# Performance work log

Measured on AMD Instinct MI355X. Metric: run time of the kernel, lower is better.

The kernel has to match this reference:

```python
import jax, jax.numpy as jnp
import numpy as np

B, N, DIM, H = 4, 3072, 768, 3  # N must be 48*64 per positional-encoding assert; H must be 3 per reshape constraint
HD = DIM // H               # 256
D = HD + 6                  # per-head dim after positional concat


def _positional(n):
    # (x^2, y^2, xy, x, y, 1) encoding over a 48x64 grid, intrinsics=None path.
    h, w = 48, 64
    ys = jnp.linspace(-1.0, 1.0, h)
    xs = jnp.linspace(-1.0, 1.0, w)
    p3 = jnp.tile(ys, w)            # [N], ys.unsqueeze(0).repeat(B, w)
    p4 = jnp.repeat(xs, h)          # [N], xs.repeat_interleave(h)
    pos = jnp.stack([p3 * p3, p4 * p4, p3 * p4, p3, p4, jnp.ones_like(p3)], axis=-1)  # [N,6]
    return pos


def setup_inputs() -> dict:
    key = jax.random.key(0)
    k0, k1, k2 = jax.random.split(key, 3)
    x = jax.random.normal(k0, (B, N, DIM), dtype=jnp.float32)
    W_qkv = jax.random.normal(k1, (3 * DIM, DIM), dtype=jnp.float32) * (DIM ** -0.5)
    W_pf = jax.random.normal(k2, (DIM, DIM + 6 * H), dtype=jnp.float32) * ((DIM + 6 * H) ** -0.5)
    b_pf = jnp.zeros((DIM,), dtype=jnp.float32)
    return {"x": x, "W_qkv": W_qkv, "W_pf": W_pf, "b_pf": b_pf}


def reference(x, W_qkv, W_pf, b_pf):
    Bb, Nn, C = x.shape
    scale = HD ** -0.5
    qkv = (x @ W_qkv.T).reshape(Bb, Nn, 3, H, HD).transpose(2, 0, 3, 1, 4)  # [3,B,H,N,hd]
    q, k, v = qkv[0], qkv[1], qkv[2]
    attn = jnp.einsum('bhnd,bhmd->bhnm', q, k) * scale          # [B,H,N,N]
    attn_f = jax.nn.softmax(attn, axis=-1) * jax.nn.softmax(attn, axis=-2)
    pos = _positional(Nn)                                       # [N,6]
    pos_b = jnp.broadcast_to(pos[None, None], (Bb, H, Nn, 6))
    v_cat = jnp.concatenate([v, pos_b], axis=-1)                # [B,H,N,D]
    # fundamental = v^T @ attn_f @ v  -> [B,H,D,D]
    f1 = jnp.einsum('bhnd,bhnm->bhdm', v_cat, attn_f)
    fund = jnp.einsum('bhdm,bhme->bhde', f1, v_cat)
    # reshape [B,H,D,D] -> [B, 3D, D] -> transpose -> [B, D, 3D]
    fund = fund.reshape(Bb, H * D, D).transpose(0, 2, 1)
    out = fund @ W_pf.T + b_pf                                  # [B, D, DIM]
    return out
```

## Files before the change

### kernel.cpp

```cpp
#include <hip/hip_runtime.h>

typedef unsigned short u16;
typedef u16 u16x8 __attribute__((ext_vector_type(8)));
typedef u16 u16x4 __attribute__((ext_vector_type(4)));
typedef __bf16 bf16x8 __attribute__((ext_vector_type(8)));
typedef float f32x4 __attribute__((ext_vector_type(4)));

#define Bn   4
#define Nn   3072
#define DIMn 768
#define Hn   3
#define HDn  256
#define BHn  12
#define Dn   262
#define EP   272
#define MSn  8
#define FP   264

__device__ __forceinline__ u16 f2bf(float f) {
    unsigned u = __builtin_bit_cast(unsigned, f);
    u += 0x7fffu + ((u >> 16) & 1u);
    return (u16)(u >> 16);
}
__device__ __forceinline__ float bf2f(u16 h) {
    unsigned u = ((unsigned)h) << 16;
    return __builtin_bit_cast(float, u);
}
__device__ __forceinline__ bf16x8 ld_frag16(const u16* p) {
    return *(const bf16x8*)p;
}
#define MFMA(a,b,c) __builtin_amdgcn_mfma_f32_16x16x32_bf16(a, b, c, 0, 0, 0)

__global__ void to_bf16(const float* __restrict__ in, u16* __restrict__ out, int n8) {
    int i = blockIdx.x * blockDim.x + threadIdx.x;
    if (i >= n8) return;
    float4 a = *(const float4*)(in + (size_t)i*8);
    float4 b = *(const float4*)(in + (size_t)i*8 + 4);
    u16x8 o;
    o[0]=f2bf(a.x); o[1]=f2bf(a.y); o[2]=f2bf(a.z); o[3]=f2bf(a.w);
    o[4]=f2bf(b.x); o[5]=f2bf(b.y); o[6]=f2bf(b.z); o[7]=f2bf(b.w);
    *(u16x8*)(out + (size_t)i*8) = o;
}

__global__ __launch_bounds__(256) void transpose_wpf(const float* __restrict__ Wpf,
                                                     float* __restrict__ WpfT) {
    __shared__ float tile[32][33];
    int jt = blockIdx.x * 32;
    int ot = blockIdx.y * 32;
    int tx = threadIdx.x & 31, ty = threadIdx.x >> 5;
    #pragma unroll
    for (int k = 0; k < 4; ++k) {
        int o = ot + ty + 8*k;
        int j = jt + tx;
        tile[ty + 8*k][tx] = (j < 786) ? Wpf[(size_t)o*786 + j] : 0.0f;
    }
    __syncthreads();
    #pragma unroll
    for (int k = 0; k < 4; ++k) {
        int j = jt + ty + 8*k;
        if (j < 786) WpfT[(size_t)j*768 + ot + tx] = tile[tx][ty + 8*k];
    }
}

__global__ __launch_bounds__(256) void qkv_mfma(const u16* __restrict__ xb,
                                                const u16* __restrict__ Wb,
                                                u16* __restrict__ qh,
                                                u16* __restrict__ kh,
                                                u16* __restrict__ vT) {
    __shared__ u16 Pool[2*128*72];
    u16* Xs = Pool;
    u16* Ws = Pool + 128*72;
    int tid = threadIdx.x;
    int w = tid >> 6, lane = tid & 63, quad = lane >> 4, l15 = lane & 15;
    int cb = blockIdx.x, rb = blockIdx.y;
    int r0 = rb * 128;
    int b_ = rb / 24;
    int n0 = (rb % 24) * 128;
    int which = cb / 6;
    int c0l = (cb % 6) * 128;
    int h = c0l >> 8, hd0 = c0l & 255;
    int bh = b_ * Hn + h;
    int wr = w >> 1, wc = w & 1;
    const u16* xp = xb + (size_t)r0*DIMn;
    const u16* wp = Wb + (size_t)(which*768 + c0l)*DIMn;
    const int sr = tid >> 3, ssg = tid & 7;

    u16x8 xreg[4], wreg[4];
    #pragma unroll
    for (int i = 0; i < 4; ++i) {
        xreg[i] = *(const u16x8*)(xp + (size_t)(sr + 32*i)*DIMn + ssg*8);
        wreg[i] = *(const u16x8*)(wp + (size_t)(sr + 32*i)*DIMn + ssg*8);
    }

    f32x4 acc[4][4];
    #pragma unroll
    for (int i = 0; i < 4; ++i)
        #pragma unroll
        for (int j = 0; j < 4; ++j) acc[i][j] = (f32x4){0.f,0.f,0.f,0.f};

    for (int k0 = 0; k0 < DIMn; k0 += 64) {
        int k0n = (k0 + 64 < DIMn) ? k0 + 64 : 0;
        __syncthreads();
        #pragma unroll
        for (int i = 0; i < 4; ++i) {
            *(u16x8*)&Xs[(sr + 32*i)*72 + ssg*8] = xreg[i];
            *(u16x8*)&Ws[(sr + 32*i)*72 + ssg*8] = wreg[i];
        }
        __syncthreads();
        #pragma unroll
        for (int i = 0; i < 4; ++i) {
            xreg[i] = *(const u16x8*)(xp + (size_t)(sr + 32*i)*DIMn + k0n + ssg*8);
            wreg[i] = *(const u16x8*)(wp + (size_t)(sr + 32*i)*DIMn + k0n + ssg*8);
        }
        #pragma unroll
        for (int ks = 0; ks < 2; ++ks) {
            bf16x8 af[4], bf[4];
            #pragma unroll
            for (int mt = 0; mt < 4; ++mt)
                af[mt] = ld_frag16(&Xs[(wr*64 + mt*16 + l15)*72 + ks*32 + quad*8]);
            #pragma unroll
            for (int nt = 0; nt < 4; ++nt)
                bf[nt] = ld_frag16(&Ws[(wc*64 + nt*16 + l15)*72 + ks*32 + quad*8]);
            #pragma unroll
            for (int mt = 0; mt < 4; ++mt)
                #pragma unroll
                for (int nt = 0; nt < 4; ++nt)
                    acc[mt][nt] = MFMA(af[mt], bf[nt], acc[mt][nt]);
        }
    }
    __syncthreads();
    u16* Cw = Pool + w*(64*72);
    if (which < 2) {
        #pragma unroll
        for (int mt = 0; mt < 4; ++mt)
            #pragma unroll
            for (int nt = 0; nt < 4; ++nt)
                #pragma unroll
                for (int r = 0; r < 4; ++r)
                    Cw[(mt*16 + quad*4 + r)*72 + nt*16 + l15] = f2bf(acc[mt][nt][r]);
    } else {
        #pragma unroll
        for (int mt = 0; mt < 4; ++mt)
            #pragma unroll
            for (int nt = 0; nt < 4; ++nt) {
                u16x4 pk;
                #pragma unroll
                for (int r = 0; r < 4; ++r) pk[r] = f2bf(acc[mt][nt][r]);
                *(u16x4*)&Cw[(nt*16 + l15)*72 + mt*16 + quad*4] = pk;
            }
    }
    __syncthreads();
    #pragma unroll
    for (int i = 0; i < 8; ++i) {
        int u = tid + i*256;
        int row = u >> 4, seg = u & 15;
        if (which < 2) {
            int wv = ((row >> 6) << 1) | (seg >> 3);
            u16x8 vv = *(const u16x8*)&Pool[wv*(64*72) + (row & 63)*72 + (seg & 7)*8];
            u16* dst = (which == 0) ? qh : kh;
            *(u16x8*)(dst + ((size_t)bh*Nn + n0 + row)*HDn + hd0 + seg*8) = vv;
        } else {
            int wv = ((seg >> 3) << 1) | (row >> 6);
            u16x8 vv = *(const u16x8*)&Pool[wv*(64*72) + (row & 63)*72 + (seg & 7)*8];
            *(u16x8*)(vT + ((size_t)bh*EP + hd0 + row)*Nn + n0 + seg*8) = vv;
        }
    }
}

__global__ void pos_fill(u16* __restrict__ vT) {
    int idx = blockIdx.x * blockDim.x + threadIdx.x;
    int bh = idx / (16*Nn);
    int rem = idx - bh*16*Nn;
    int row = rem / Nn;
    int n = rem - row*Nn;
    int gy = n % 48, gx = n / 48;
    float p3 = -1.0f + (2.0f/47.0f)*gy;
    float p4 = -1.0f + (2.0f/63.0f)*gx;
    float v = 0.f;
    if (row == 0) v = p3*p3;
    else if (row == 1) v = p4*p4;
    else if (row == 2) v = p3*p4;
    else if (row == 3) v = p3;
    else if (row == 4) v = p4;
    else if (row == 5) v = 1.0f;
    vT[((size_t)bh*EP + 256 + row)*Nn + n] = f2bf(v);
}

__global__ __launch_bounds__(256) void rc_mfma(const u16* __restrict__ qh,
                                               const u16* __restrict__ kh,
                                               float* __restrict__ R_part,
                                               float* __restrict__ C_part,
                                               u16* __restrict__ P2,
                                               int g0) {
    __shared__ u16 Ks[64*264];
    __shared__ float rbuf[2][2][64];
    int tid = threadIdx.x;
    int w = tid >> 6, lane = tid & 63, quad = lane >> 4, l15 = lane & 15;
    int bhl = blockIdx.z;
    int bh = g0 + bhl;
    int nb = blockIdx.y;
    int n0 = nb * 64;
    int ms = blockIdx.x;
    int msBase = ms * (Nn/MSn);
    const u16* qp = qh + ((size_t)bh*Nn + n0)*HDn;
    const u16* kp = kh + (size_t)bh*Nn*HDn;
    u16* pw = P2 + (size_t)bhl*Nn*Nn;
    int wm = w & 1, wn = w >> 1;

    #pragma unroll
    for (int i = 0; i < 8; ++i) {
        int e = tid + i*256;
        int row = e >> 5, seg = e & 31;
        *(u16x8*)&Ks[row*264 + seg*8] = *(const u16x8*)(qp + (size_t)row*HDn + seg*8);
    }
    __syncthreads();
    bf16x8 qf[2][8];
    #pragma unroll
    for (int nt = 0; nt < 2; ++nt)
        #pragma unroll
        for (int ks = 0; ks < 8; ++ks)
            qf[nt][ks] = ld_frag16(&Ks[((2*wn+nt)*16 + l15)*264 + ks*32 + quad*8]);

    const int kr = tid >> 5, ksg = tid & 31;
    u16x8 kreg[8];
    #pragma unroll
    for (int i = 0; i < 8; ++i)
        kreg[i] = *(const u16x8*)(kp + (size_t)(msBase + kr + 8*i)*HDn + ksg*8);

    float* cpart = C_part + ((size_t)(nb*2 + wn)*BHn + bh)*Nn;
    float rAcc[2] = {0.f, 0.f};
    const int NCH = Nn/(MSn*64);
    for (int mc = 0; mc < NCH; ++mc) {
        int m0 = msBase + mc*64;
        int m0n = msBase + ((mc + 1 < NCH) ? (mc + 1)*64 : 0);
        __syncthreads();
        #pragma unroll
        for (int i = 0; i < 8; ++i)
            *(u16x8*)&Ks[(kr + 8*i)*264 + ksg*8] = kreg[i];
        __syncthreads();
        #pragma unroll
        for (int i = 0; i < 8; ++i)
            kreg[i] = *(const u16x8*)(kp + (size_t)(m0n + kr + 8*i)*HDn + ksg*8);
        f32x4 sacc[2][2];
        #pragma unroll
        for (int i = 0; i < 2; ++i)
            #pragma unroll
            for (int j = 0; j < 2; ++j) sacc[i][j] = (f32x4){0.f,0.f,0.f,0.f};
        #pragma unroll
        for (int ks = 0; ks < 8; ++ks) {
            bf16x8 a0 = ld_frag16(&Ks[((2*wm+0)*16 + l15)*264 + ks*32 + quad*8]);
            bf16x8 a1 = ld_frag16(&Ks[((2*wm+1)*16 + l15)*264 + ks*32 + quad*8]);
            sacc[0][0] = MFMA(a0, qf[0][ks], sacc[0][0]);
            sacc[0][1] = MFMA(a0, qf[1][ks], sacc[0][1]);
            sacc[1][0] = MFMA(a1, qf[0][ks], sacc[1][0]);
            sacc[1][1] = MFMA(a1, qf[1][ks], sacc[1][1]);
        }
        float ex[2][2][4];
        #pragma unroll
        for (int mt = 0; mt < 2; ++mt)
            #pragma unroll
            for (int nt = 0; nt < 2; ++nt)
                #pragma unroll
                for (int r = 0; r < 4; ++r)
                    ex[mt][nt][r] = __expf(0.0625f * sacc[mt][nt][r]);
        #pragma unroll
        for (int mt = 0; mt < 2; ++mt)
            #pragma unroll
            for (int nt = 0; nt < 2; ++nt) {
                u16x4 pk;
                #pragma unroll
                for (int r = 0; r < 4; ++r) {
                    float e2 = ex[mt][nt][r];
                    pk[r] = f2bf(e2 * e2);
                }
                *(u16x4*)(pw + (size_t)(n0 + (2*wn+nt)*16 + l15)*Nn
                             + m0 + (2*wm+mt)*16 + quad*4) = pk;
            }
        #pragma unroll
        for (int nt = 0; nt < 2; ++nt)
            #pragma unroll
            for (int mt = 0; mt < 2; ++mt)
                #pragma unroll
                for (int r = 0; r < 4; ++r) rAcc[nt] += ex[mt][nt][r];
        {
            float v0 = ex[0][0][0] + ex[0][1][0];
            float v1 = ex[0][0][1] + ex[0][1][1];
            float v2 = ex[0][0][2] + ex[0][1][2];
            float v3 = ex[0][0][3] + ex[0][1][3];
            float v4 = ex[1][0][0] + ex[1][1][0];
            float v5 = ex[1][0][1] + ex[1][1][1];
            float v6 = ex[1][0][2] + ex[1][1][2];
            float v7 = ex[1][0][3] + ex[1][1][3];
            int b0 = l15 & 1, b1 = l15 & 2, b2 = l15 & 4;
            float u01 = (b0 ? v1 : v0) + __shfl_xor(b0 ? v0 : v1, 1, 16);
            float u23 = (b0 ? v3 : v2) + __shfl_xor(b0 ? v2 : v3, 1, 16);
            float u45 = (b0 ? v5 : v4) + __shfl_xor(b0 ? v4 : v5, 1, 16);
            float u67 = (b0 ? v7 : v6) + __shfl_xor(b0 ? v6 : v7, 1, 16);
            float t03 = (b1 ? u23 : u01) + __shfl_xor(b1 ? u01 : u23, 2, 16);
            float t47 = (b1 ? u67 : u45) + __shfl_xor(b1 ? u45 : u67, 2, 16);
            float s07 = (b2 ? t47 : t03) + __shfl_xor(b2 ? t03 : t47, 4, 16);
            s07 += __shfl_xor(s07, 8, 16);
            if (l15 < 8)
                cpart[m0 + (2*wm + (l15 >> 2))*16 + quad*4 + (l15 & 3)] = s07;
        }
    }
    #pragma unroll
    for (int nt = 0; nt < 2; ++nt) {
        float rp = rAcc[nt];
        rp += __shfl_xor(rp, 16, 64);
        rp += __shfl_xor(rp, 32, 64);
        if (quad == 0) rbuf[wm][nt][wn*32 + l15] = rp;
    }
    __syncthreads();
    #pragma unroll
    for (int nt = 0; nt < 2; ++nt) {
        if (quad == 0 && wm == 0) {
            float tot = rbuf[0][nt][wn*32 + l15] + rbuf[1][nt][wn*32 + l15];
            R_part[(size_t)ms*BHn*Nn + (size_t)bh*Nn + n0 + (2*wn+nt)*16 + l15] = tot;
        }
    }
}

__global__ void inv_kernel(const float* __restrict__ Rg,
                           const float* __restrict__ Cg,
                           float* __restrict__ iRg, float* __restrict__ iCg) {
    int i = blockIdx.x * blockDim.x + threadIdx.x;
    float r = 0.f;
    #pragma unroll
    for (int s = 0; s < MSn; ++s)
        r += Rg[(size_t)s*BHn*Nn + i];
    float c = 0.f;
    for (int s = 0; s < 96; ++s)
        c += Cg[(size_t)s*BHn*Nn + i];
    iRg[i] = 1.0f / r;
    iCg[i] = 1.0f / c;
}

__global__ void scale_v(const u16* __restrict__ vTg, const float* __restrict__ iCg,
                        u16* __restrict__ vTs) {
    int idx = blockIdx.x * blockDim.x + threadIdx.x;
    int bhl = idx / (EP*Nn/8);
    int rem = idx - bhl*(EP*Nn/8);
    size_t off = (size_t)bhl*EP*Nn + (size_t)rem*8;
    int m = (rem % (Nn/8)) * 8;
    u16x8 v = *(const u16x8*)(vTg + off);
    float4 c0 = *(const float4*)(iCg + (size_t)bhl*Nn + m);
    float4 c1 = *(const float4*)(iCg + (size_t)bhl*Nn + m + 4);
    u16x8 o;
    o[0]=f2bf(bf2f(v[0])*c0.x); o[1]=f2bf(bf2f(v[1])*c0.y);
    o[2]=f2bf(bf2f(v[2])*c0.z); o[3]=f2bf(bf2f(v[3])*c0.w);
    o[4]=f2bf(bf2f(v[4])*c1.x); o[5]=f2bf(bf2f(v[5])*c1.y);
    o[6]=f2bf(bf2f(v[6])*c1.z); o[7]=f2bf(bf2f(v[7])*c1.w);
    *(u16x8*)(vTs + off) = o;
}

__global__ __launch_bounds__(256, 4) void pv_mfma(const u16* __restrict__ P2,
                                                  const u16* __restrict__ vTs,
                                                  const float* __restrict__ iRg,
                                                  u16* __restrict__ f1aTg) {
    __shared__ u16 Ps2[64*72];
    __shared__ u16 Vt[144*72];
    int tid = threadIdx.x;
    int w = tid >> 6, lane = tid & 63, quad = lane >> 4, l15 = lane & 15;
    int bhl = blockIdx.y, n0 = blockIdx.x * 64;
    int z = blockIdx.z;
    const u16* pp = P2  + ((size_t)bhl*Nn + n0)*Nn;
    const u16* vp = vTs + (size_t)bhl*EP*Nn + (size_t)(z*128)*Nn;
    const int sr = tid >> 3, sg = tid & 7;
    u16x8 preg[2], vreg[5];
    #pragma unroll
    for (int i = 0; i < 2; ++i)
        preg[i] = *(const u16x8*)(pp + (size_t)(sr + 32*i)*Nn + sg*8);
    #pragma unroll
    for (int i = 0; i < 5; ++i)
        if (i < 4 || (z == 1 && tid < 128))
            vreg[i] = *(const u16x8*)(vp + (size_t)(sr + 32*i)*Nn + sg*8);

    f32x4 acc[4][3];
    #pragma unroll
    for (int a = 0; a < 4; ++a)
        #pragma unroll
        for (int b = 0; b < 3; ++b) acc[a][b] = (f32x4){0.f,0.f,0.f,0.f};

    for (int mc = 0; mc < Nn/64; ++mc) {
        int m0n = (mc + 1 < Nn/64) ? (mc + 1)*64 : 0;
        __syncthreads();
        #pragma unroll
        for (int i = 0; i < 2; ++i)
            *(u16x8*)&Ps2[(sr + 32*i)*72 + sg*8] = preg[i];
        #pragma unroll
        for (int i = 0; i < 5; ++i)
            if (i < 4 || (z == 1 && tid < 128))
                *(u16x8*)&Vt[(sr + 32*i)*72 + sg*8] = vreg[i];
        __syncthreads();
        #pragma unroll
        for (int i = 0; i < 2; ++i)
            preg[i] = *(const u16x8*)(pp + (size_t)(sr + 32*i)*Nn + m0n + sg*8);
        #pragma unroll
        for (int i = 0; i < 5; ++i)
            if (i < 4 || (z == 1 && tid < 128))
                vreg[i] = *(const u16x8*)(vp + (size_t)(sr + 32*i)*Nn + m0n + sg*8);
        #pragma unroll
        for (int ks = 0; ks < 2; ++ks) {
            bf16x8 pa[4];
            #pragma unroll
            for (int nt = 0; nt < 4; ++nt)
                pa[nt] = ld_frag16(&Ps2[(nt*16 + l15)*72 + ks*32 + quad*8]);
            #pragma unroll
            for (int et = 0; et < 3; ++et) {
                const int lt = (et < 2) ? (w*2 + et) : 8;
                const bool act = (et < 2 || (z == 1 && w == 3));
                if (act) {
                    bf16x8 vb = ld_frag16(&Vt[(lt*16 + l15)*72 + ks*32 + quad*8]);
                    #pragma unroll
                    for (int nt = 0; nt < 4; ++nt)
                        acc[nt][et] = MFMA(pa[nt], vb, acc[nt][et]);
                }
            }
        }
    }
    #pragma unroll
    for (int nt = 0; nt < 4; ++nt) {
        float4 ir4 = *(const float4*)(iRg + (size_t)bhl*Nn + n0 + nt*16 + quad*4);
        #pragma unroll
        for (int et = 0; et < 3; ++et) {
            const int tile = (et < 2) ? (z*8 + w*2 + et) : 16;
            const bool act = (et < 2 || (z == 1 && w == 3));
            if (act) {
                int e = tile*16 + l15;
                u16x4 ov;
                #pragma unroll
                for (int r = 0; r < 4; ++r)
                    ov[r] = f2bf(acc[nt][et][r] * ((const float*)&ir4)[r]);
                *(u16x4*)(f1aTg + ((size_t)bhl*EP + e)*Nn + n0 + nt*16 + quad*4) = ov;
            }
        }
    }
}

__global__ __launch_bounds__(256) void fund_mfma(const u16* __restrict__ vT,
                                                 const u16* __restrict__ f1aT,
                                                 float* __restrict__ fund) {
    __shared__ u16 At[64*136];
    __shared__ u16 Bt[64*136];
    int tid = threadIdx.x;
    int w = tid >> 6, lane = tid & 63, quad = lane >> 4, l15 = lane & 15;
    int bh = blockIdx.z;
    int d0 = blockIdx.y * 64, e0 = blockIdx.x * 64;
    const u16* ap = vT   + (size_t)bh*EP*Nn;
    const u16* bp = f1aT + (size_t)bh*EP*Nn;
    int wd = w & 1, we = w >> 1;
    const u16x8 zero8 = {0,0,0,0,0,0,0,0};

    f32x4 acc[2][2];
    #pragma unroll
    for (int i = 0; i < 2; ++i)
        #pragma unroll
        for (int j = 0; j < 2; ++j) acc[i][j] = (f32x4){0.f,0.f,0.f,0.f};

    for (int nc = 0; nc < Nn; nc += 128) {
        __syncthreads();
        #pragma unroll
        for (int i = 0; i < 4; ++i) {
            int u = tid + i*256;
            int row = u >> 4, seg = u & 15;
            int da = d0 + row, eb = e0 + row;
            *(u16x8*)&At[row*136 + seg*8] = (da < EP)
                ? *(const u16x8*)(ap + (size_t)da*Nn + nc + seg*8) : zero8;
            *(u16x8*)&Bt[row*136 + seg*8] = (eb < EP)
                ? *(const u16x8*)(bp + (size_t)eb*Nn + nc + seg*8) : zero8;
        }
        __syncthreads();
        #pragma unroll
        for (int ks = 0; ks < 4; ++ks) {
            bf16x8 a0 = ld_frag16(&At[((2*wd+0)*16 + l15)*136 + ks*32 + quad*8]);
            bf16x8 a1 = ld_frag16(&At[((2*wd+1)*16 + l15)*136 + ks*32 + quad*8]);
            bf16x8 b0 = ld_frag16(&Bt[((2*we+0)*16 + l15)*136 + ks*32 + quad*8]);
            bf16x8 b1 = ld_frag16(&Bt[((2*we+1)*16 + l15)*136 + ks*32 + quad*8]);
            acc[0][0] = MFMA(a0, b0, acc[0][0]);
            acc[0][1] = MFMA(a0, b1, acc[0][1]);
            acc[1][0] = MFMA(a1, b0, acc[1][0]);
            acc[1][1] = MFMA(a1, b1, acc[1][1]);
        }
    }
    #pragma unroll
    for (int dt = 0; dt < 2; ++dt)
        #pragma unroll
        for (int et = 0; et < 2; ++et)
            #pragma unroll
            for (int r = 0; r < 4; ++r) {
                int d = d0 + (2*wd+dt)*16 + quad*4 + r;
                int e = e0 + (2*we+et)*16 + l15;
                if (d < Dn && e < Dn)
                    fund[(size_t)bh*Dn*FP + (size_t)d*FP + e] = acc[dt][et][r];
            }
}

__global__ __launch_bounds__(256) void out_gemm(const float* __restrict__ fund,
                                                const float* __restrict__ WpfT,
                                                const float* __restrict__ bpf,
                                                float* __restrict__ out) {
    __shared__ float As[2][16][68];
    __shared__ float Bs[2][16][68];
    int tid = threadIdx.x;
    int b_ = blockIdx.z;
    int d2b = blockIdx.y * 64, ob = blockIdx.x * 64;
    int ty = tid >> 4, tx = tid & 15;
    int srow = tid >> 4, sc4 = (tid & 15) * 4;
    const int NIT = (786 + 15) / 16;

    float4 aReg, bReg;
    {
        int j = srow;
        aReg = (float4){0.f,0.f,0.f,0.f};
        bReg = (float4){0.f,0.f,0.f,0.f};
        int h = j / Dn, d1 = j - h*Dn;
        const float* srcA = fund + ((size_t)(b_*Hn + h)*Dn + d1)*FP + d2b + sc4;
        if (d2b + sc4 + 3 < Dn) aReg = *(const float4*)srcA;
        else {
            float t[4] = {0.f,0.f,0.f,0.f};
            for (int u2 = 0; u2 < 4; ++u2)
                if (d2b + sc4 + u2 < Dn) t[u2] = srcA[u2];
            aReg = (float4){t[0],t[1],t[2],t[3]};
        }
        bReg = *(const float4*)(WpfT + (size_t)j*768 + ob + sc4);
    }
    *(float4*)&As[0][srow][sc4] = aReg;
    *(float4*)&Bs[0][srow][sc4] = bReg;
    __syncthreads();

    float acc[4][4] = {};
    for (int c = 0; c < NIT; ++c) {
        int buf = c & 1;
        if (c + 1 < NIT) {
            int j = (c + 1)*16 + srow;
            aReg = (float4){0.f,0.f,0.f,0.f};
            bReg = (float4){0.f,0.f,0.f,0.f};
            if (j < 786) {
                int h = j / Dn, d1 = j - h*Dn;
                const float* srcA = fund + ((size_t)(b_*Hn + h)*Dn + d1)*FP + d2b + sc4;
                if (d2b + sc4 + 3 < Dn) aReg = *(const float4*)srcA;
                else {
                    float t[4] = {0.f,0.f,0.f,0.f};
                    for (int u2 = 0; u2 < 4; ++u2)
                        if (d2b + sc4 + u2 < Dn) t[u2] = srcA[u2];
                    aReg = (float4){t[0],t[1],t[2],t[3]};
                }
                bReg = *(const float4*)(WpfT + (size_t)j*768 + ob + sc4);
            }
        }
        #pragma unroll
        for (int kk = 0; kk < 16; ++kk) {
            float4 a = *(const float4*)&As[buf][kk][ty*4];
            float4 b = *(const float4*)&Bs[buf][kk][tx*4];
            acc[0][0] += a.x*b.x; acc[0][1] += a.x*b.y; acc[0][2] += a.x*b.z; acc[0][3] += a.x*b.w;
            acc[1][0] += a.y*b.x; acc[1][1] += a.y*b.y; acc[1][2] += a.y*b.z; acc[1][3] += a.y*b.w;
            acc[2][0] += a.z*b.x; acc[2][1] += a.z*b.y; acc[2][2] += a.z*b.z; acc[2][3] += a.z*b.w;
            acc[3][0] += a.w*b.x; acc[3][1] += a.w*b.y; acc[3][2] += a.w*b.z; acc[3][3] += a.w*b.w;
        }
        if (c + 1 < NIT) {
            *(float4*)&As[buf^1][srow][sc4] = aReg;
            *(float4*)&Bs[buf^1][srow][sc4] = bReg;
            __syncthreads();
        }
    }
    #pragma unroll
    for (int i = 0; i < 4; ++i) {
        int d2 = d2b + ty*4 + i;
        if (d2 >= Dn) continue;
        #pragma unroll
        for (int j = 0; j < 4; ++j) {
            int o = ob + tx*4 + j;
            out[((size_t)b_*Dn + d2)*DIMn + o] = acc[i][j] + bpf[o];
        }
    }
}

extern "C" void kernel_launch(void* const* d_in, const int* in_sizes, int n_in,
                              void* d_out, int out_size, void* d_ws, size_t ws_size,
                              hipStream_t stream) {
    const float* x    = (const float*)d_in[0];
    const float* Wqkv = (const float*)d_in[1];
    const float* Wpf  = (const float*)d_in[2];
    const float* bpf  = (const float*)d_in[3];
    float* out = (float*)d_out;

    char* p = (char*)d_ws;
    u16* qh    = (u16*)p;                       p += (size_t)BHn*Nn*HDn*2;
    u16* kh    = (u16*)p;                       p += (size_t)BHn*Nn*HDn*2;
    u16* vT    = (u16*)p;                       p += (size_t)BHn*EP*Nn*2;
    u16* f1aT  = (u16*)p;                       p += (size_t)BHn*EP*Nn*2;
    float* Cp  = (float*)p;                     p += (size_t)96*BHn*Nn*4;
    float* iR  = (float*)p;                     p += (size_t)BHn*Nn*4;
    float* iC  = (float*)p;                     p += (size_t)BHn*Nn*4;
    float* fund= (float*)p;                     p += (size_t)BHn*Dn*FP*4 + 256;
    float* WpfT= (float*)p;                     p += (size_t)786*768*4;
    char* region2 = p;
    size_t fixedB = (size_t)(region2 - (char*)d_ws);
    size_t avail = (ws_size > fixedB) ? (ws_size - fixedB) : 0;

    const size_t perBh = ((size_t)Nn*Nn + (size_t)EP*Nn) * 2;
    const size_t rpB   = (size_t)MSn*BHn*Nn*4;
    int gbh = 1;
    const int cand[5] = {12, 6, 4, 3, 2};
    for (int ci = 0; ci < 5; ++ci) {
        if ((size_t)cand[ci]*perBh + rpB <= avail) { gbh = cand[ci]; break; }
    }

    u16* xb = (u16*)region2;
    u16* Wb = xb + (size_t)Bn*Nn*DIMn;
    u16* P2  = (u16*)region2;
    u16* vTs = P2 + (size_t)gbh*Nn*Nn;
    float* Rp = (float*)(vTs + (size_t)gbh*EP*Nn);

    to_bf16  <<<dim3((Bn*Nn*DIMn/8 + 255)/256), 256, 0, stream>>>(x, xb, Bn*Nn*DIMn/8);
    to_bf16  <<<dim3((3*DIMn*DIMn/8 + 255)/256), 256, 0, stream>>>(Wqkv, Wb, 3*DIMn*DIMn/8);
    transpose_wpf<<<dim3(25, 24), 256, 0, stream>>>(Wpf, WpfT);
    qkv_mfma <<<dim3(18, 96), 256, 0, stream>>>(xb, Wb, qh, kh, vT);
    pos_fill <<<dim3(BHn*16*Nn/256), 256, 0, stream>>>(vT);

    for (int g0 = 0; g0 < BHn; g0 += gbh) {
        rc_mfma  <<<dim3(MSn, Nn/64, gbh), 256, 0, stream>>>(qh, kh, Rp, Cp, P2, g0);
        inv_kernel<<<dim3(gbh*Nn/256), 256, 0, stream>>>(
            Rp + (size_t)g0*Nn, Cp + (size_t)g0*Nn, iR + (size_t)g0*Nn, iC + (size_t)g0*Nn);
        scale_v  <<<dim3(gbh*EP*Nn/8/256), 256, 0, stream>>>(
            vT + (size_t)g0*EP*Nn, iC + (size_t)g0*Nn, vTs);
        pv_mfma  <<<dim3(Nn/64, gbh, 2), 256, 0, stream>>>(
            P2, vTs, iR + (size_t)g0*Nn, f1aT + (size_t)g0*EP*Nn);
    }

    fund_mfma<<<dim3(5, 5, BHn), 256, 0, stream>>>(vT, f1aT, fund);
    out_gemm <<<dim3(DIMn/64, 5, Bn), 256, 0, stream>>>(fund, WpfT, bpf, out);
}
```

Before: 545.9 us.

## Split-K fund_mfma across four N slices with register-prefetched tiles, reduce in out_gemm

The fund GEMM now splits its 3072-long reduction into four slices, so the grid grows from 300 to 1200 blocks and fills the GPU better. Each slice writes its own partial result buffer, and out_gemm sums the four partials as it loads its A operand. The main loop also prefetches the next global tile into registers while the MFMAs run on the current shared-memory tile. The cost is four times the fund workspace, extra global traffic for the partials, and extra loads in out_gemm.

Result: faster. 525.3 us (-3.8%).

```diff
diff --git a/kernel.cpp b/kernel.cpp
--- a/kernel.cpp
+++ b/kernel.cpp
@@ -16,6 +16,7 @@
 #define EP   272
 #define MSn  8
 #define FP   264
+#define KSn  4
 
 __device__ __forceinline__ u16 f2bf(float f) {
     unsigned u = __builtin_bit_cast(unsigned, f);
@@ -440,17 +441,31 @@
 
 __global__ __launch_bounds__(256) void fund_mfma(const u16* __restrict__ vT,
                                                  const u16* __restrict__ f1aT,
-                                                 float* __restrict__ fund) {
+                                                 float* __restrict__ fund_part) {
     __shared__ u16 At[64*136];
     __shared__ u16 Bt[64*136];
     int tid = threadIdx.x;
     int w = tid >> 6, lane = tid & 63, quad = lane >> 4, l15 = lane & 15;
-    int bh = blockIdx.z;
+    int bz = blockIdx.z;
+    int bh = bz >> 2;
+    int ks = bz & 3;
     int d0 = blockIdx.y * 64, e0 = blockIdx.x * 64;
     const u16* ap = vT   + (size_t)bh*EP*Nn;
     const u16* bp = f1aT + (size_t)bh*EP*Nn;
     int wd = w & 1, we = w >> 1;
     const u16x8 zero8 = {0,0,0,0,0,0,0,0};
+    const int nc0 = ks * (Nn/KSn);
+    const int NCH = (Nn/KSn)/128;
+
+    const int srow = tid >> 4, seg = tid & 15;
+    u16x8 areg[4], breg[4];
+    #pragma unroll
+    for (int i = 0; i < 4; ++i) {
+        int row = srow + 16*i;
+        int da = d0 + row, eb = e0 + row;
+        areg[i] = (da < EP) ? *(const u16x8*)(ap + (size_t)da*Nn + nc0 + seg*8) : zero8;
+        breg[i] = (eb < EP) ? *(const u16x8*)(bp + (size_t)eb*Nn + nc0 + seg*8) : zero8;
+    }
 
     f32x4 acc[2][2];
     #pragma unroll
@@ -458,31 +473,36 @@
         #pragma unroll
         for (int j = 0; j < 2; ++j) acc[i][j] = (f32x4){0.f,0.f,0.f,0.f};
 
-    for (int nc = 0; nc < Nn; nc += 128) {
+    for (int mc = 0; mc < NCH; ++mc) {
+        int ncn = nc0 + ((mc + 1 < NCH) ? (mc + 1)*128 : 0);
         __syncthreads();
         #pragma unroll
         for (int i = 0; i < 4; ++i) {
-            int u = tid + i*256;
-            int row = u >> 4, seg = u & 15;
+            int row = srow + 16*i;
+            *(u16x8*)&At[row*136 + seg*8] = areg[i];
+            *(u16x8*)&Bt[row*136 + seg*8] = breg[i];
+        }
+        __syncthreads();
+        #pragma unroll
+        for (int i = 0; i < 4; ++i) {
+            int row = srow + 16*i;
             int da = d0 + row, eb = e0 + row;
-            *(u16x8*)&At[row*136 + seg*8] = (da < EP)
-                ? *(const u16x8*)(ap + (size_t)da*Nn + nc + seg*8) : zero8;
-            *(u16x8*)&Bt[row*136 + seg*8] = (eb < EP)
-                ? *(const u16x8*)(bp + (size_t)eb*Nn + nc + seg*8) : zero8;
-        }
-        __syncthreads();
-        #pragma unroll
-        for (int ks = 0; ks < 4; ++ks) {
-            bf16x8 a0 = ld_frag16(&At[((2*wd+0)*16 + l15)*136 + ks*32 + quad*8]);
-            bf16x8 a1 = ld_frag16(&At[((2*wd+1)*16 + l15)*136 + ks*32 + quad*8]);
-            bf16x8 b0 = ld_frag16(&Bt[((2*we+0)*16 + l15)*136 + ks*32 + quad*8]);
-            bf16x8 b1 = ld_frag16(&Bt[((2*we+1)*16 + l15)*136 + ks*32 + quad*8]);
+            areg[i] = (da < EP) ? *(const u16x8*)(ap + (size_t)da*Nn + ncn + seg*8) : zero8;
+            breg[i] = (eb < EP) ? *(const u16x8*)(bp + (size_t)eb*Nn + ncn + seg*8) : zero8;
+        }
+        #pragma unroll
+        for (int kk = 0; kk < 4; ++kk) {
+            bf16x8 a0 = ld_frag16(&At[((2*wd+0)*16 + l15)*136 + kk*32 + quad*8]);
+            bf16x8 a1 = ld_frag16(&At[((2*wd+1)*16 + l15)*136 + kk*32 + quad*8]);
+            bf16x8 b0 = ld_frag16(&Bt[((2*we+0)*16 + l15)*136 + kk*32 + quad*8]);
+            bf16x8 b1 = ld_frag16(&Bt[((2*we+1)*16 + l15)*136 + kk*32 + quad*8]);
             acc[0][0] = MFMA(a0, b0, acc[0][0]);
             acc[0][1] = MFMA(a0, b1, acc[0][1]);
             acc[1][0] = MFMA(a1, b0, acc[1][0]);
             acc[1][1] = MFMA(a1, b1, acc[1][1]);
         }
     }
+    float* fp = fund_part + (size_t)(ks*BHn + bh)*Dn*FP;
     #pragma unroll
     for (int dt = 0; dt < 2; ++dt)
         #pragma unroll
@@ -492,16 +512,26 @@
                 int d = d0 + (2*wd+dt)*16 + quad*4 + r;
                 int e = e0 + (2*we+et)*16 + l15;
                 if (d < Dn && e < Dn)
-                    fund[(size_t)bh*Dn*FP + (size_t)d*FP + e] = acc[dt][et][r];
+                    fp[(size_t)d*FP + e] = acc[dt][et][r];
             }
 }
 
-__global__ __launch_bounds__(256) void out_gemm(const float* __restrict__ fund,
+__device__ __forceinline__ float4 ld4sum(const float* p, size_t SL) {
+    float4 a = *(const float4*)p;
+    float4 b = *(const float4*)(p + SL);
+    float4 c = *(const float4*)(p + 2*SL);
+    float4 d = *(const float4*)(p + 3*SL);
+    return (float4){a.x+b.x+c.x+d.x, a.y+b.y+c.y+d.y,
+                    a.z+b.z+c.z+d.z, a.w+b.w+c.w+d.w};
+}
+
+__global__ __launch_bounds__(256) void out_gemm(const float* __restrict__ fund_part,
                                                 const float* __restrict__ WpfT,
                                                 const float* __restrict__ bpf,
                                                 float* __restrict__ out) {
     __shared__ float As[2][16][68];
     __shared__ float Bs[2][16][68];
+    const size_t SL = (size_t)BHn*Dn*FP;
     int tid = threadIdx.x;
     int b_ = blockIdx.z;
     int d2b = blockIdx.y * 64, ob = blockIdx.x * 64;
@@ -512,15 +542,14 @@
     float4 aReg, bReg;
     {
         int j = srow;
-        aReg = (float4){0.f,0.f,0.f,0.f};
-        bReg = (float4){0.f,0.f,0.f,0.f};
         int h = j / Dn, d1 = j - h*Dn;
-        const float* srcA = fund + ((size_t)(b_*Hn + h)*Dn + d1)*FP + d2b + sc4;
-        if (d2b + sc4 + 3 < Dn) aReg = *(const float4*)srcA;
+        const float* srcA = fund_part + ((size_t)(b_*Hn + h)*Dn + d1)*FP + d2b + sc4;
+        if (d2b + sc4 + 3 < Dn) aReg = ld4sum(srcA, SL);
         else {
             float t[4] = {0.f,0.f,0.f,0.f};
             for (int u2 = 0; u2 < 4; ++u2)
-                if (d2b + sc4 + u2 < Dn) t[u2] = srcA[u2];
+                if (d2b + sc4 + u2 < Dn)
+                    t[u2] = srcA[u2] + srcA[u2+SL] + srcA[u2+2*SL] + srcA[u2+3*SL];
             aReg = (float4){t[0],t[1],t[2],t[3]};
         }
         bReg = *(const float4*)(WpfT + (size_t)j*768 + ob + sc4);
@@ -538,12 +567,13 @@
             bReg = (float4){0.f,0.f,0.f,0.f};
             if (j < 786) {
                 int h = j / Dn, d1 = j - h*Dn;
-                const float* srcA = fund + ((size_t)(b_*Hn + h)*Dn + d1)*FP + d2b + sc4;
-                if (d2b + sc4 + 3 < Dn) aReg = *(const float4*)srcA;
+                const float* srcA = fund_part + ((size_t)(b_*Hn + h)*Dn + d1)*FP + d2b + sc4;
+                if (d2b + sc4 + 3 < Dn) aReg = ld4sum(srcA, SL);
                 else {
                     float t[4] = {0.f,0.f,0.f,0.f};
                     for (int u2 = 0; u2 < 4; ++u2)
-                        if (d2b + sc4 + u2 < Dn) t[u2] = srcA[u2];
+                        if (d2b + sc4 + u2 < Dn)
+                            t[u2] = srcA[u2] + srcA[u2+SL] + srcA[u2+2*SL] + srcA[u2+3*SL];
                     aReg = (float4){t[0],t[1],t[2],t[3]};
                 }
                 bReg = *(const float4*)(WpfT + (size_t)j*768 + ob + sc4);
@@ -593,7 +623,7 @@
     float* Cp  = (float*)p;                     p += (size_t)96*BHn*Nn*4;
     float* iR  = (float*)p;                     p += (size_t)BHn*Nn*4;
     float* iC  = (float*)p;                     p += (size_t)BHn*Nn*4;
-    float* fund= (float*)p;                     p += (size_t)BHn*Dn*FP*4 + 256;
+    float* fund= (float*)p;                     p += (size_t)KSn*BHn*Dn*FP*4 + 256;
     float* WpfT= (float*)p;                     p += (size_t)786*768*4;
     char* region2 = p;
     size_t fixedB = (size_t)(region2 - (char*)d_ws);
@@ -629,6 +659,6 @@
             P2, vTs, iR + (size_t)g0*Nn, f1aT + (size_t)g0*EP*Nn);
     }
 
-    fund_mfma<<<dim3(5, 5, BHn), 256, 0, stream>>>(vT, f1aT, fund);
+    fund_mfma<<<dim3(5, 5, BHn*KSn), 256, 0, stream>>>(vT, f1aT, fund);
     out_gemm <<<dim3(DIMn/64, 5, Bn), 256, 0, stream>>>(fund, WpfT, bpf, out);
 }
```
